# Optimization experiments

Hardware: AMD Instinct MI355X
Metric: run time of the kernel (lower is better)

Reference implementation:

```python
import jax, jax.numpy as jnp
import numpy as np

EPSILON = 0.1


def setup_inputs() -> dict:
    key = jax.random.key(0)
    ks = jax.random.split(key, 6)
    N, E, F_IN, F_OUT, NF = 50000, 800000, 256, 96, 3
    x = jax.random.normal(ks[0], (N, F_IN), dtype=jnp.float32)
    adj_vals = jax.random.uniform(ks[1], (E,), dtype=jnp.float32)
    d_scales = jax.random.uniform(ks[2], (NF, N), dtype=jnp.float32)
    # xavier-uniform-ish weights
    limit = np.sqrt(6.0 / (F_IN + F_OUT)).astype(np.float32)
    weights = jax.random.uniform(ks[3], (NF, F_IN, F_OUT), dtype=jnp.float32,
                                 minval=-limit, maxval=limit)
    bias = jnp.zeros((F_OUT,), dtype=jnp.float32)
    edge_index = jax.random.randint(ks[4], (2, E), 0, N, dtype=jnp.int32)
    return {"x": x, "adj_vals": adj_vals, "d_scales": d_scales,
            "weights": weights, "bias": bias, "edge_index": edge_index}


def reference(x, adj_vals, d_scales, weights, bias, edge_index):
    N = x.shape[0]
    row, col = edge_index[0], edge_index[1]

    # degree with self loops (add_remaining_self_loops adds 1 per node)
    deg = jax.ops.segment_sum(jnp.ones_like(adj_vals), row, num_segments=N) + 1.0
    eps_deg_inv = EPSILON / deg  # [N], diagonal of sparse_degree(..., epsilon)

    def spmm(t):  # symadj @ t via edge list
        return jax.ops.segment_sum(adj_vals[:, None] * t[col], row, num_segments=N)

    out = jnp.zeros((N, weights.shape[2]), dtype=x.dtype)
    n_filters = weights.shape[0]
    for ii in range(n_filters):
        sign = -1.0 if ii == 0 else 1.0  # Ad = symadj -/+ eps*diag(deg^-1)
        t = d_scales[ii][:, None] * (x @ weights[ii])          # D @ (x W)
        t = spmm(t) + sign * eps_deg_inv[:, None] * t          # Ad @ t
        t = d_scales[ii][:, None] * jax.nn.relu(t)             # D @ relu(t)
        out = out + t
    return out + bias
```

## Files before the change

kernel.cpp:

```cpp
#include <hip/hip_runtime.h>

#define EPSILON 0.1f
#define F_IN 256
#define F_OUT 96
#define NF 3
#define TCOLS 288
#define TSTRIDE 320
#define CAP 64
#define BN 96
#define CW 104
#define NCVT (TCOLS * F_IN / 4)

#define RPB 64
#define NBINS 782
#define BCAP 1536
#define EPB 2048
#define GPAD 32

typedef __attribute__((ext_vector_type(8))) short bf8_t;
typedef __attribute__((ext_vector_type(4))) float f32x4;

__device__ inline ushort f2b(float f) {
    union { float f; unsigned u; } v; v.f = f;
    unsigned u = v.u;
    return (ushort)((u + 0x7FFFu + ((u >> 16) & 1u)) >> 16);
}
__device__ inline float blo(unsigned u) { return __uint_as_float(u << 16); }
__device__ inline float bhi(unsigned u) { return __uint_as_float(u & 0xffff0000u); }

__device__ inline bf8_t cvt8(float4 a, float4 b) {
    bf8_t r;
    r[0] = (short)f2b(a.x); r[1] = (short)f2b(a.y);
    r[2] = (short)f2b(a.z); r[3] = (short)f2b(a.w);
    r[4] = (short)f2b(b.x); r[5] = (short)f2b(b.y);
    r[6] = (short)f2b(b.z); r[7] = (short)f2b(b.w);
    return r;
}

__global__ __launch_bounds__(256) void setup_kernel(const float* __restrict__ w,
                                                    ushort* __restrict__ wt,
                                                    int* __restrict__ gcur) {
    int tid = blockIdx.x * 256 + threadIdx.x;
    if (tid < NCVT) {
        int base = tid * 4;
        int gc = base >> 8;
        int k  = base & 255;
        int ii = gc / F_OUT;
        int c  = gc - ii * F_OUT;
        const float* wp = w + (size_t)ii * (F_IN * F_OUT) + (size_t)k * F_OUT + c;
        ushort4 o;
        o.x = f2b(wp[0 * F_OUT]);
        o.y = f2b(wp[1 * F_OUT]);
        o.z = f2b(wp[2 * F_OUT]);
        o.w = f2b(wp[3 * F_OUT]);
        *(ushort4*)(wt + base) = o;
    } else {
        int z = (tid - NCVT) * 4;
        if (z + 3 < NBINS * GPAD) {
            *(int4*)(gcur + z) = make_int4(0, 0, 0, 0);
        }
    }
}

__global__ __launch_bounds__(256) void bin_cvt_kernel(
        const int* __restrict__ row, const int* __restrict__ col,
        const float* __restrict__ vals, int E,
        int* __restrict__ gcur, int2* __restrict__ gout,
        const float* __restrict__ x, ushort* __restrict__ xb, int N, int nbin) {
    __shared__ int hist[NBINS];
    __shared__ int gbase[NBINS];

    if ((int)blockIdx.x < nbin) {
        int tid = threadIdx.x;
        for (int i = tid; i < NBINS; i += 256) hist[i] = 0;
        __syncthreads();

        int e0 = (int)blockIdx.x * EPB;
        int4 r4[2], c4[2]; float4 v4[2];
        int rank[8], binv[8], valv[8];
        unsigned recx[8];
        #pragma unroll
        for (int g = 0; g < 2; ++g) {
            int e = e0 + tid * 4 + g * 1024;
            if (e + 3 < E) {
                r4[g] = *(const int4*)(row + e);
                c4[g] = *(const int4*)(col + e);
                v4[g] = *(const float4*)(vals + e);
            } else {
                int4 rr, cc; float4 vv;
                int* rp = (int*)&rr; int* cp = (int*)&cc; float* vp = (float*)&vv;
                #pragma unroll
                for (int j = 0; j < 4; ++j) {
                    int ee = e + j;
                    rp[j] = (ee < E) ? row[ee] : -1;
                    cp[j] = (ee < E) ? col[ee] : 0;
                    vp[j] = (ee < E) ? vals[ee] : 0.f;
                }
                r4[g] = rr; c4[g] = cc; v4[g] = vv;
            }
        }
        #pragma unroll
        for (int g = 0; g < 2; ++g) {
            const int* rp = (const int*)&r4[g];
            const int* cp = (const int*)&c4[g];
            const float* vp = (const float*)&v4[g];
            #pragma unroll
            for (int j = 0; j < 4; ++j) {
                int s = g * 4 + j;
                int r = rp[j];
                if (r >= 0) {
                    int b = r >> 6;
                    binv[s] = b;
                    recx[s] = (unsigned)(cp[j] & 0xffff) |
                              ((unsigned)(r & 63) << 16) | ((unsigned)b << 22);
                    valv[s] = __float_as_int(vp[j]);
                    rank[s] = atomicAdd(&hist[b], 1);
                } else {
                    binv[s] = -1; rank[s] = 0; recx[s] = 0; valv[s] = 0;
                }
            }
        }
        __syncthreads();

        #pragma unroll
        for (int q = 0; q < 4; ++q) {
            int i = threadIdx.x * 4 + q;
            if (i < NBINS) {
                int h = hist[i];
                gbase[i] = h ? atomicAdd(&gcur[i * GPAD], h) : 0;
            }
        }
        __syncthreads();

        #pragma unroll
        for (int s = 0; s < 8; ++s) {
            int b = binv[s];
            if (b >= 0) {
                int pos = gbase[b] + rank[s];
                if (pos < BCAP)
                    gout[(size_t)b * BCAP + pos] = make_int2((int)recx[s], valv[s]);
            }
        }
    } else {
        size_t base = ((size_t)((int)blockIdx.x - nbin) * 256 + threadIdx.x) * 8;
        if (base < (size_t)N * F_IN) {
            float4 a = *(const float4*)(x + base);
            float4 b = *(const float4*)(x + base + 4);
            bf8_t o = cvt8(a, b);
            *(bf8_t*)(xb + base) = o;
        }
    }
}

__global__ __launch_bounds__(512) void gemm_bucket(
        const ushort* __restrict__ xb, const ushort* __restrict__ wt,
        const float* __restrict__ dsc, ushort* __restrict__ t, int N,
        int nper, int nw,
        const int2* __restrict__ gout, const int* __restrict__ gcur,
        int* __restrict__ cnt, int2* __restrict__ evs2) {
    __shared__ ushort Bs[BN * F_IN];

    int tid = threadIdx.x;

    if ((int)blockIdx.x < NBINS) {
        int2* buck = (int2*)Bs;
        int*  lcnt = (int*)(Bs + 16384);
        int b = blockIdx.x;
        if (tid < RPB) lcnt[tid] = 0;
        __syncthreads();

        int nrec = gcur[b * GPAD];
        if (nrec > BCAP) nrec = BCAP;
        for (int i = tid; i < nrec; i += 512) {
            int2 rec = gout[(size_t)b * BCAP + i];
            int rl = (rec.x >> 16) & 63;
            int c  = rec.x & 0xffff;
            int k = atomicAdd(&lcnt[rl], 1);
            if (k < CAP) buck[rl * CAP + k] = make_int2(c * TSTRIDE, rec.y);
        }
        __syncthreads();

        int row0 = b * RPB;
        if (tid < RPB && row0 + tid < N) cnt[row0 + tid] = lcnt[tid];

        int lane = tid & 63, wave = tid >> 6;
        for (int r = wave; r < RPB; r += 8) {
            int rowg = row0 + r;
            if (rowg >= N) break;
            int m = min(lcnt[r], CAP);
            if (lane < m)
                evs2[(size_t)rowg * CAP + lane] = buck[r * CAP + lane];
        }
        return;
    }

    int lb = (int)blockIdx.x - NBINS;
    int xcd = lb & 7, li = lb >> 3;
    int w = xcd * nper + li;
    if (w >= nw) return;
    int mb = w / 3, cb = w - mb * 3;

    int lane = tid & 63, wave = tid >> 6;
    int cl = lane & 15, quad = lane >> 4;
    int gc0 = cb * BN;
    int m0 = mb * 128 + wave * 16;
    int mrow = m0 + cl;
    bool aok = (mrow < N);

    #pragma unroll
    for (int i = 0; i < 6; ++i) {
        int F = tid + i * 512;
        int rem = F & 63;
        int q = rem >> 4, c = rem & 15;
        int ksj = F >> 6;
        int ks = ksj / 6, j = ksj - ks * 6;
        int gc = gc0 + j * 16 + c;
        *(uint4*)(Bs + (size_t)F * 8) =
            *(const uint4*)(wt + (size_t)gc * F_IN + ks * 32 + q * 8);
    }

    uint4 areg[8];
    const ushort* xp = xb + (size_t)mrow * F_IN + quad * 8;
    const uint4 zu = make_uint4(0, 0, 0, 0);
    #pragma unroll
    for (int ks = 0; ks < 8; ++ks)
        areg[ks] = aok ? *(const uint4*)(xp + ks * 32) : zu;

    f32x4 acc[6];
    #pragma unroll
    for (int j = 0; j < 6; ++j) acc[j] = (f32x4){0.f, 0.f, 0.f, 0.f};

    __syncthreads();

    #pragma unroll
    for (int ks = 0; ks < 8; ++ks) {
        bf8_t a = *(const bf8_t*)&areg[ks];
        const ushort* bb = Bs + ((size_t)(ks * 6) * 64 + lane) * 8;
        #pragma unroll
        for (int j = 0; j < 6; ++j) {
            bf8_t b = *(const bf8_t*)(bb + j * 64 * 8);
            acc[j] = __builtin_amdgcn_mfma_f32_16x16x32_bf16(a, b, acc[j], 0, 0, 0);
        }
    }

    __syncthreads();
    ushort* Cw = Bs + wave * (16 * CW);
    float dscv[3][4];
    #pragma unroll
    for (int ii = 0; ii < 3; ++ii)
        #pragma unroll
        for (int r = 0; r < 4; ++r) {
            int rowg = m0 + quad * 4 + r;
            dscv[ii][r] = (rowg < N) ? dsc[(size_t)ii * N + rowg] : 0.f;
        }
    #pragma unroll
    for (int j = 0; j < 6; ++j) {
        int ii = (gc0 + j * 16) / F_OUT;
        #pragma unroll
        for (int r = 0; r < 4; ++r)
            Cw[(quad * 4 + r) * CW + j * 16 + cl] = f2b(dscv[ii][r] * acc[j][r]);
    }
    #pragma unroll
    for (int it = 0; it < 3; ++it) {
        int idx = lane + it * 64;
        int r = idx / 12, ch = idx - r * 12;
        int grow = m0 + r;
        if (grow < N)
            *(uint4*)(t + (size_t)grow * TSTRIDE + gc0 + ch * 8) =
                *(const uint4*)&Cw[r * CW + ch * 8];
    }
}

__device__ inline void acc8(float* acc, uint4 a, float v) {
    acc[0] = fmaf(v, blo(a.x), acc[0]); acc[1] = fmaf(v, bhi(a.x), acc[1]);
    acc[2] = fmaf(v, blo(a.y), acc[2]); acc[3] = fmaf(v, bhi(a.y), acc[3]);
    acc[4] = fmaf(v, blo(a.z), acc[4]); acc[5] = fmaf(v, bhi(a.z), acc[5]);
    acc[6] = fmaf(v, blo(a.w), acc[6]); acc[7] = fmaf(v, bhi(a.w), acc[7]);
}

__global__ __launch_bounds__(256) void spmm_kernel(const ushort* __restrict__ t,
                                                   const int2* __restrict__ evs2,
                                                   const int* __restrict__ cnt,
                                                   const float* __restrict__ dsc,
                                                   const float* __restrict__ bias,
                                                   float* __restrict__ out, int N) {
    int lane = threadIdx.x & 63;
    int wave = threadIdx.x >> 6;
    int n = blockIdx.x * 4 + wave;
    if (n >= N) return;

    int deg = cnt[n];
    int mm = (deg < CAP) ? deg : CAP;
    int s = n * CAP, e = s + mm;
    int coff = (lane < 40) ? lane * 8 : 0;

    float acc[8];
    #pragma unroll
    for (int j = 0; j < 8; ++j) acc[j] = 0.f;

    for (int base = s; base < e; base += 64) {
        int idx = base + lane;
        int2 q = make_int2(0, 0);
        if (idx < e) q = evs2[idx];
        int m = min(64, e - base);
        int j = 0;
        for (; j + 3 < m; j += 4) {
            int c0 = __shfl(q.x, j, 64);
            int c1 = __shfl(q.x, j + 1, 64);
            int c2 = __shfl(q.x, j + 2, 64);
            int c3 = __shfl(q.x, j + 3, 64);
            float v0 = __int_as_float(__shfl(q.y, j, 64));
            float v1 = __int_as_float(__shfl(q.y, j + 1, 64));
            float v2 = __int_as_float(__shfl(q.y, j + 2, 64));
            float v3 = __int_as_float(__shfl(q.y, j + 3, 64));
            uint4 a0 = *(const uint4*)(t + (size_t)c0 + coff);
            uint4 a1 = *(const uint4*)(t + (size_t)c1 + coff);
            uint4 a2 = *(const uint4*)(t + (size_t)c2 + coff);
            uint4 a3 = *(const uint4*)(t + (size_t)c3 + coff);
            acc8(acc, a0, v0);
            acc8(acc, a1, v1);
            acc8(acc, a2, v2);
            acc8(acc, a3, v3);
        }
        for (; j < m; ++j) {
            int c = __shfl(q.x, j, 64);
            float v = __int_as_float(__shfl(q.y, j, 64));
            uint4 a = *(const uint4*)(t + (size_t)c + coff);
            acc8(acc, a, v);
        }
    }

    float sign = (lane < 12) ? -1.f : 1.f;
    float epsdi = EPSILON / (float)(deg + 1);
    int ii = lane / 12;
    float dscv = (lane < 36) ? dsc[(size_t)ii * N + n] : 0.f;
    uint4 sv = *(const uint4*)(t + (size_t)n * TSTRIDE + coff);
    float se = sign * epsdi;
    float val[8];
    {
        unsigned u;
        u = sv.x; val[0] = fmaf(se, blo(u), acc[0]); val[1] = fmaf(se, bhi(u), acc[1]);
        u = sv.y; val[2] = fmaf(se, blo(u), acc[2]); val[3] = fmaf(se, bhi(u), acc[3]);
        u = sv.z; val[4] = fmaf(se, blo(u), acc[4]); val[5] = fmaf(se, bhi(u), acc[5]);
        u = sv.w; val[6] = fmaf(se, blo(u), acc[6]); val[7] = fmaf(se, bhi(u), acc[7]);
    }
    #pragma unroll
    for (int j = 0; j < 8; ++j) val[j] = fmaxf(val[j], 0.f) * dscv;

    float res[8];
    #pragma unroll
    for (int j = 0; j < 8; ++j) {
        float r1 = __shfl(val[j], lane + 12, 64);
        float r2 = __shfl(val[j], lane + 24, 64);
        res[j] = val[j] + r1 + r2;
    }
    if (lane < 12) {
        float4 b0 = *(const float4*)(bias + lane * 8);
        float4 b1 = *(const float4*)(bias + lane * 8 + 4);
        float4 o0 = make_float4(res[0] + b0.x, res[1] + b0.y, res[2] + b0.z, res[3] + b0.w);
        float4 o1 = make_float4(res[4] + b1.x, res[5] + b1.y, res[6] + b1.z, res[7] + b1.w);
        *(float4*)(out + (size_t)n * F_OUT + lane * 8) = o0;
        *(float4*)(out + (size_t)n * F_OUT + lane * 8 + 4) = o1;
    }
}

extern "C" void kernel_launch(void* const* d_in, const int* in_sizes, int n_in,
                              void* d_out, int out_size, void* d_ws, size_t ws_size,
                              hipStream_t stream) {
    const float* x    = (const float*)d_in[0];
    const float* adj  = (const float*)d_in[1];
    const float* dsc  = (const float*)d_in[2];
    const float* w    = (const float*)d_in[3];
    const float* bias = (const float*)d_in[4];
    const int*   ei   = (const int*)d_in[5];

    int E = in_sizes[1];
    int N = in_sizes[0] / F_IN;
    const int* row = ei;
    const int* col = ei + E;
    float* out = (float*)d_out;

    char* p = (char*)d_ws;
    auto take = [&](size_t bytes) {
        char* r = p;
        p += (bytes + 255) & ~(size_t)255;
        return r;
    };
    int*    cnt  = (int*)take((size_t)N * 4);
    int2*   evs2 = (int2*)take((size_t)N * CAP * 8);
    ushort* wt   = (ushort*)take((size_t)TCOLS * F_IN * 2);
    ushort* xb   = (ushort*)take((size_t)N * F_IN * 2);
    ushort* t    = (ushort*)take(((size_t)N * TSTRIDE + 256) * 2);
    int*    gcur = (int*)take((size_t)NBINS * GPAD * 4);
    int2*   gout = (int2*)take((size_t)NBINS * BCAP * 8);

    int nzero = (NBINS * GPAD + 3) / 4;
    setup_kernel<<<(NCVT + nzero + 255) / 256, 256, 0, stream>>>(w, wt, gcur);

    int nbin  = (E + EPB - 1) / EPB;
    int ncvtx = ((N * F_IN / 8) + 255) / 256;
    bin_cvt_kernel<<<nbin + ncvtx, 256, 0, stream>>>(row, col, adj, E, gcur, gout,
                                                     x, xb, N, nbin);

    int nt = (N + 127) / 128;
    int nw = 3 * nt;
    int nper = (((nw + 7) / 8) + 2) / 3 * 3;
    gemm_bucket<<<NBINS + 8 * nper, 512, 0, stream>>>(xb, wt, dsc, t, N, nper, nw,
                                                      gout, gcur, cnt, evs2);
    spmm_kernel<<<(N + 3) / 4, 256, 0, stream>>>(t, evs2, cnt, dsc, bias, out, N);
}
```

Measured before the change: 220.6 us.

## Fold weight conversion into bin kernel, shrink t stride, pad LDS buckets

Removes the separate setup kernel: the gcur counters are now zeroed with hipMemsetAsync and the weight bf16 conversion runs as extra blocks of bin_cvt_kernel. The intermediate t row stride drops from 320 to 288, which cuts the memory footprint and gather traffic in spmm. LDS bucket rows are padded to 65 entries to avoid bank conflicts. The GEMM epilogue now loads only the one d_scale row its column block needs. These are several unrelated small changes bundled into one commit.

```diff
diff --git a/kernel.cpp b/kernel.cpp
--- a/kernel.cpp
+++ b/kernel.cpp
@@ -5,7 +5,7 @@
 #define F_OUT 96
 #define NF 3
 #define TCOLS 288
-#define TSTRIDE 320
+#define TSTRIDE 288
 #define CAP 64
 #define BN 96
 #define CW 104
@@ -16,6 +16,7 @@
 #define BCAP 1536
 #define EPB 2048
 #define GPAD 32
+#define BPAD 65
 
 typedef __attribute__((ext_vector_type(8))) short bf8_t;
 typedef __attribute__((ext_vector_type(4))) float f32x4;
@@ -37,36 +38,13 @@
     return r;
 }
 
-__global__ __launch_bounds__(256) void setup_kernel(const float* __restrict__ w,
-                                                    ushort* __restrict__ wt,
-                                                    int* __restrict__ gcur) {
-    int tid = blockIdx.x * 256 + threadIdx.x;
-    if (tid < NCVT) {
-        int base = tid * 4;
-        int gc = base >> 8;
-        int k  = base & 255;
-        int ii = gc / F_OUT;
-        int c  = gc - ii * F_OUT;
-        const float* wp = w + (size_t)ii * (F_IN * F_OUT) + (size_t)k * F_OUT + c;
-        ushort4 o;
-        o.x = f2b(wp[0 * F_OUT]);
-        o.y = f2b(wp[1 * F_OUT]);
-        o.z = f2b(wp[2 * F_OUT]);
-        o.w = f2b(wp[3 * F_OUT]);
-        *(ushort4*)(wt + base) = o;
-    } else {
-        int z = (tid - NCVT) * 4;
-        if (z + 3 < NBINS * GPAD) {
-            *(int4*)(gcur + z) = make_int4(0, 0, 0, 0);
-        }
-    }
-}
-
 __global__ __launch_bounds__(256) void bin_cvt_kernel(
         const int* __restrict__ row, const int* __restrict__ col,
         const float* __restrict__ vals, int E,
         int* __restrict__ gcur, int2* __restrict__ gout,
-        const float* __restrict__ x, ushort* __restrict__ xb, int N, int nbin) {
+        const float* __restrict__ x, ushort* __restrict__ xb, int N,
+        const float* __restrict__ w, ushort* __restrict__ wt,
+        int nbin, int ncvt) {
     __shared__ int hist[NBINS];
     __shared__ int gbase[NBINS];
 
@@ -141,13 +119,29 @@
                     gout[(size_t)b * BCAP + pos] = make_int2((int)recx[s], valv[s]);
             }
         }
-    } else {
+    } else if ((int)blockIdx.x < nbin + ncvt) {
         size_t base = ((size_t)((int)blockIdx.x - nbin) * 256 + threadIdx.x) * 8;
         if (base < (size_t)N * F_IN) {
             float4 a = *(const float4*)(x + base);
             float4 b = *(const float4*)(x + base + 4);
             bf8_t o = cvt8(a, b);
             *(bf8_t*)(xb + base) = o;
+        }
+    } else {
+        int tid = ((int)blockIdx.x - nbin - ncvt) * 256 + threadIdx.x;
+        if (tid < NCVT) {
+            int base = tid * 4;
+            int gc = base >> 8;
+            int k  = base & 255;
+            int ii = gc / F_OUT;
+            int c  = gc - ii * F_OUT;
+            const float* wp = w + (size_t)ii * (F_IN * F_OUT) + (size_t)k * F_OUT + c;
+            ushort4 o;
+            o.x = f2b(wp[0 * F_OUT]);
+            o.y = f2b(wp[1 * F_OUT]);
+            o.z = f2b(wp[2 * F_OUT]);
+            o.w = f2b(wp[3 * F_OUT]);
+            *(ushort4*)(wt + base) = o;
         }
     }
 }
@@ -164,7 +158,7 @@
 
     if ((int)blockIdx.x < NBINS) {
         int2* buck = (int2*)Bs;
-        int*  lcnt = (int*)(Bs + 16384);
+        int*  lcnt = (int*)(Bs + 16768);
         int b = blockIdx.x;
         if (tid < RPB) lcnt[tid] = 0;
         __syncthreads();
@@ -176,7 +170,7 @@
             int rl = (rec.x >> 16) & 63;
             int c  = rec.x & 0xffff;
             int k = atomicAdd(&lcnt[rl], 1);
-            if (k < CAP) buck[rl * CAP + k] = make_int2(c * TSTRIDE, rec.y);
+            if (k < CAP) buck[rl * BPAD + k] = make_int2(c * TSTRIDE, rec.y);
         }
         __syncthreads();
 
@@ -189,7 +183,7 @@
             if (rowg >= N) break;
             int m = min(lcnt[r], CAP);
             if (lane < m)
-                evs2[(size_t)rowg * CAP + lane] = buck[r * CAP + lane];
+                evs2[(size_t)rowg * CAP + lane] = buck[r * BPAD + lane];
         }
         return;
     }
@@ -245,20 +239,17 @@
 
     __syncthreads();
     ushort* Cw = Bs + wave * (16 * CW);
-    float dscv[3][4];
-    #pragma unroll
-    for (int ii = 0; ii < 3; ++ii)
-        #pragma unroll
-        for (int r = 0; r < 4; ++r) {
-            int rowg = m0 + quad * 4 + r;
-            dscv[ii][r] = (rowg < N) ? dsc[(size_t)ii * N + rowg] : 0.f;
-        }
+    float dscr[4];
+    #pragma unroll
+    for (int r = 0; r < 4; ++r) {
+        int rowg = m0 + quad * 4 + r;
+        dscr[r] = (rowg < N) ? dsc[(size_t)cb * N + rowg] : 0.f;
+    }
     #pragma unroll
     for (int j = 0; j < 6; ++j) {
-        int ii = (gc0 + j * 16) / F_OUT;
         #pragma unroll
         for (int r = 0; r < 4; ++r)
-            Cw[(quad * 4 + r) * CW + j * 16 + cl] = f2b(dscv[ii][r] * acc[j][r]);
+            Cw[(quad * 4 + r) * CW + j * 16 + cl] = f2b(dscr[r] * acc[j][r]);
     }
     #pragma unroll
     for (int it = 0; it < 3; ++it) {
@@ -292,7 +283,7 @@
     int deg = cnt[n];
     int mm = (deg < CAP) ? deg : CAP;
     int s = n * CAP, e = s + mm;
-    int coff = (lane < 40) ? lane * 8 : 0;
+    int coff = (lane < 36) ? lane * 8 : 0;
 
     float acc[8];
     #pragma unroll
@@ -394,13 +385,13 @@
     int*    gcur = (int*)take((size_t)NBINS * GPAD * 4);
     int2*   gout = (int2*)take((size_t)NBINS * BCAP * 8);
 
-    int nzero = (NBINS * GPAD + 3) / 4;
-    setup_kernel<<<(NCVT + nzero + 255) / 256, 256, 0, stream>>>(w, wt, gcur);
+    hipMemsetAsync(gcur, 0, (size_t)NBINS * GPAD * 4, stream);
 
     int nbin  = (E + EPB - 1) / EPB;
     int ncvtx = ((N * F_IN / 8) + 255) / 256;
-    bin_cvt_kernel<<<nbin + ncvtx, 256, 0, stream>>>(row, col, adj, E, gcur, gout,
-                                                     x, xb, N, nbin);
+    int nwt   = (NCVT + 255) / 256;
+    bin_cvt_kernel<<<nbin + ncvtx + nwt, 256, 0, stream>>>(
+        row, col, adj, E, gcur, gout, x, xb, N, w, wt, nbin, ncvtx);
 
     int nt = (N + 127) / 128;
     int nw = 3 * nt;
```

New measurement: 218.1 us. No clear change (-1.1%).
